# Kernel optimization log

Hardware: AMD Instinct MI355X
Metric: run time of the kernel (lower is better)

## Reference

```python
import jax, jax.numpy as jnp
import numpy as np
from jax import lax

TABLE_SIZE = 1024   # LSH table buckets
R = 2.5             # hash bucket width r
U = 0.83            # ALSH norm rescale bound
M = 9               # appended ALSH dims; M // (K*K) = 1 extra channel
K = 3               # kernel spatial size
PAD = 1


def _P(kflat, m):
    # L2-ALSH preprocessing: rescale so max row norm == U, append ||x||^{2^i}, i=1..m
    norms = jnp.linalg.norm(kflat, axis=1)
    x = kflat * (U / jnp.max(norms))
    p = jnp.sum(x * x, axis=1)  # ||x||^2
    powers = [p]
    for _ in range(m - 1):
        powers.append(powers[-1] ** 2)
    return jnp.concatenate([x, jnp.stack(powers, axis=1)], axis=1)  # [O, D+m]


def _conv(x, w):
    return lax.conv_general_dilated(
        x, w, window_strides=(1, 1), padding=[(PAD, PAD), (PAD, PAD)],
        dimension_numbers=("NCHW", "OIHW", "NCHW"))


def setup_inputs() -> dict:
    key = jax.random.key(0)
    k1, k2, k3, k4 = jax.random.split(key, 4)
    inp = jax.random.normal(k1, (16, 128, 64, 64), jnp.float32)
    kernels = jax.random.normal(k2, (256, 128, 3, 3), jnp.float32) * 0.05
    d = 128 + M // (K * K)  # 129
    a = jax.random.normal(k3, (d * K * K,), jnp.float32)  # 1161
    b = jax.random.uniform(k4, (1,), jnp.float32) * R
    return {"input": inp, "kernels": kernels, "a": a, "b": b}


def reference(input, kernels, a, b):
    O, C, kh, kw = kernels.shape
    B, _, H, W = input.shape
    extra_ch = M // (kh * kw)
    d = C + extra_ch

    # ---- init_table: hash every kernel row into a bucket ----
    kflat = kernels.reshape(O, -1)                       # [O, C*kh*kw]
    h = jnp.floor((_P(kflat, M) @ a + b[0]) / R)         # [O]
    bucket = jnp.abs(jnp.fmod(h.astype(jnp.int32), TABLE_SIZE))  # torch fmod+abs semantics

    # ---- vote: Q appends 0.5-filled channels, conv with hash vector as kernel ----
    input_Q = jnp.concatenate(
        [input, jnp.full((B, extra_ch, H, W), 0.5, input.dtype)], axis=1)
    dotted = _conv(input_Q, a.reshape(1, d, kh, kw))     # [B,1,H,W]
    votes = jnp.floor((dotted.reshape(-1) + b[0]) / R).astype(jnp.int32)
    vbucket = jnp.abs(jnp.fmod(votes, TABLE_SIZE))

    # ---- count_votes + argmax bucket ----
    count = jax.ops.segment_sum(jnp.ones(vbucket.shape, jnp.float32),
                                vbucket, num_segments=TABLE_SIZE)
    index = jnp.argmax(count)

    # ---- active set: kernels whose table bucket == winning bucket (mask form, jit-safe) ----
    mask = (bucket == index)                             # [O] bool
    active_kernels = kernels * mask[:, None, None, None].astype(kernels.dtype)

    # apply the active set (the conv this module feeds downstream)
    out = _conv(input, active_kernels)                   # [B,O,H,W]
    return out, index, mask
```

## Files before the change

### kernel.cpp

```cpp
#include <hip/hip_runtime.h>
#include <cmath>
#include <cstdint>

#define TSZ 1024
#define RDIV 2.5f
#define UCONST 0.83f

typedef __bf16 bf16x8 __attribute__((ext_vector_type(8)));
typedef float f32x4 __attribute__((ext_vector_type(4)));
typedef unsigned short ushortT;

__device__ __forceinline__ ushortT bf16r(float f) {
  union { float f; unsigned u; } x; x.f = f;
  unsigned r = (x.u + 0x7FFFu + ((x.u >> 16) & 1u)) >> 16;
  return (ushortT)r;
}

__device__ __forceinline__ void glds16(const void* g, void* l) {
  __builtin_amdgcn_global_load_lds(
      (const __attribute__((address_space(1))) unsigned int*)(g),
      (__attribute__((address_space(3))) unsigned int*)(l), 16, 0, 0);
}

__global__ __launch_bounds__(256) void k_cvtg(const float* __restrict__ in,
                                              const float* __restrict__ a,
                                              ushortT* __restrict__ nb,
                                              float* __restrict__ g) {
  __shared__ float tile2[64][129];
  __shared__ float gpart[4][9][64];
  const int bid = blockIdx.x;
  const int n = bid >> 6, y = bid & 63;
  const int t = threadIdx.x;
  {
    const int chs = t >> 4, l16 = t & 15;
    const float* basep = in + ((size_t)(n * 128) << 12) + (y << 6) + (l16 << 2);
#pragma unroll
    for (int i = 0; i < 8; ++i) {
      int ch = (i << 4) + chs;
      f32x4 v = *reinterpret_cast<const f32x4*>(basep + ((size_t)ch << 12));
#pragma unroll
      for (int u = 0; u < 4; ++u) tile2[(l16 << 2) + u][ch] = v[u];
    }
  }
  __syncthreads();
  {
    const int part = __builtin_amdgcn_readfirstlane(t >> 6);
    const int x = t & 63;
    float gacc[9];
#pragma unroll
    for (int tap = 0; tap < 9; ++tap) gacc[tap] = 0.f;
    const int c0 = part << 5;
#pragma unroll
    for (int i = 0; i < 32; ++i) {
      float v = tile2[x][c0 + i];
      const float* ap = a + (c0 + i) * 9;
#pragma unroll
      for (int tap = 0; tap < 9; ++tap) gacc[tap] += v * ap[tap];
    }
#pragma unroll
    for (int tap = 0; tap < 9; ++tap) gpart[part][tap][x] = gacc[tap];
  }
  __syncthreads();
  if (t < 64) {
    const int x = t;
#pragma unroll
    for (int tap = 0; tap < 9; ++tap) {
      float s = gpart[0][tap][x] + gpart[1][tap][x] + gpart[2][tap][x] + gpart[3][tap][x];
      g[tap * 65536 + (n << 12) + (y << 6) + x] = s;
    }
  }
  {
    const int x2 = t >> 2;
    ushortT* dst = nb + (((size_t)((n << 6) + y) << 6) + x2) * 128;
#pragma unroll
    for (int j = 0; j < 4; ++j) {
      int c0 = ((t & 3) << 3) + (j << 5);
      union { ushortT us[8]; uint4 v; } pk;
#pragma unroll
      for (int u = 0; u < 8; ++u) pk.us[u] = bf16r(tile2[x2][c0 + u]);
      *reinterpret_cast<uint4*>(dst + c0) = pk.v;
    }
  }
}

__global__ __launch_bounds__(256) void k_vote3(const float* __restrict__ g,
                                               const float* __restrict__ a,
                                               const float* __restrict__ bb,
                                               int* __restrict__ count) {
  __shared__ int hist[TSZ];
  const int t = threadIdx.x;
  for (int i = t; i < TSZ; i += 256) hist[i] = 0;
  __syncthreads();
  const int pix = blockIdx.x * 256 + t;
  const int n = pix >> 12, y = (pix >> 6) & 63, x = pix & 63;
  float acc = 0.f;
#pragma unroll
  for (int tap = 0; tap < 9; ++tap) {
    const int dy = tap / 3 - 1, dx = tap % 3 - 1;
    const int yy = y + dy, xx = x + dx;
    if ((unsigned)yy < 64u && (unsigned)xx < 64u)
      acc += g[tap * 65536 + (n << 12) + (yy << 6) + xx];
  }
  {
    const float* av = a + 1152;
#pragma unroll
    for (int ky = 0; ky < 3; ++ky) {
      int yy = y + ky - 1;
      if ((unsigned)yy >= 64u) continue;
#pragma unroll
      for (int kx = 0; kx < 3; ++kx) {
        int xx = x + kx - 1;
        if ((unsigned)xx >= 64u) continue;
        acc += 0.5f * av[ky * 3 + kx];
      }
    }
  }
  int v = (int)floorf((acc + bb[0]) / RDIV);
  int r = v % TSZ; if (r < 0) r = -r;
  atomicAdd(&hist[r], 1);
  __syncthreads();
  for (int i = t; i < TSZ; i += 256) {
    int h = hist[i];
    if (h) atomicAdd(&count[i], h);
  }
}

__global__ __launch_bounds__(256) void k_norm(const float* __restrict__ k,
                                              unsigned* __restrict__ scaleBits) {
  int o = blockIdx.x;
  const float* row = k + (size_t)o * 1152;
  float s = 0.f;
  for (int j = threadIdx.x; j < 1152; j += 256) { float v = row[j]; s += v * v; }
  __shared__ float red[256];
  red[threadIdx.x] = s; __syncthreads();
  for (int st = 128; st; st >>= 1) {
    if (threadIdx.x < st) red[threadIdx.x] += red[threadIdx.x + st];
    __syncthreads();
  }
  if (threadIdx.x == 0) atomicMax(scaleBits, __float_as_uint(red[0]));
}

__global__ __launch_bounds__(256) void k_hash(const float* __restrict__ k,
                                              const float* __restrict__ a,
                                              const float* __restrict__ b,
                                              const unsigned* __restrict__ scaleBits,
                                              int* __restrict__ bucket) {
  int o = blockIdx.x;
  float scale = UCONST / sqrtf(__uint_as_float(scaleBits[0]));
  const float* row = k + (size_t)o * 1152;
  float dot = 0.f, p = 0.f;
  for (int j = threadIdx.x; j < 1152; j += 256) {
    float x = row[j] * scale;
    dot += x * a[j];
    p += x * x;
  }
  __shared__ float rd[256], rp[256];
  rd[threadIdx.x] = dot; rp[threadIdx.x] = p; __syncthreads();
  for (int st = 128; st; st >>= 1) {
    if (threadIdx.x < st) { rd[threadIdx.x] += rd[threadIdx.x + st]; rp[threadIdx.x] += rp[threadIdx.x + st]; }
    __syncthreads();
  }
  if (threadIdx.x == 0) {
    float acc = rd[0];
    float pw = rp[0];
    for (int i = 0; i < 9; i++) { acc += pw * a[1152 + i]; pw = pw * pw; }
    acc += b[0];
    float h = floorf(acc / RDIV);
    int hi = (int)h;
    int r = hi % TSZ; if (r < 0) r = -r;
    bucket[o] = r;
  }
}

__global__ __launch_bounds__(256) void k_wprep2(const int* __restrict__ count,
                                                const int* __restrict__ bucket,
                                                const float* __restrict__ w,
                                                ushortT* __restrict__ wb,
                                                float* __restrict__ tail) {
  __shared__ int sc[256];
  __shared__ int si[256];
  const int t = threadIdx.x;
  int bc = count[t], bi = t;
#pragma unroll
  for (int j = 1; j < 4; ++j) {
    int i2 = t + j * 256;
    int c2 = count[i2];
    if (c2 > bc) { bc = c2; bi = i2; }
  }
  sc[t] = bc; si[t] = bi; __syncthreads();
  for (int st = 128; st; st >>= 1) {
    if (t < st) {
      int c2 = sc[t + st], i2 = si[t + st];
      if (c2 > sc[t] || (c2 == sc[t] && i2 < si[t])) { sc[t] = c2; si[t] = i2; }
    }
    __syncthreads();
  }
  const int idx = si[0];
  const int o = blockIdx.x;
  const int m = (bucket[o] == idx) ? 1 : 0;
  if (t == 0) {
    if (o == 0) tail[0] = (float)idx;
    tail[1 + o] = (float)m;
  }
  const float mf = m ? 1.f : 0.f;
  const float* wr = w + (size_t)o * 1152;
  ushortT* dst = wb + (size_t)o * 1152;
  for (int j = t; j < 1152; j += 256) {
    int r = j >> 7, c = j & 127;
    dst[j] = bf16r(wr[c * 9 + r] * mf);
  }
}

__global__ __launch_bounds__(512, 2) void k_gemm3r(const ushortT* __restrict__ nb,
                                                   const ushortT* __restrict__ wb,
                                                   const char* __restrict__ zp,
                                                   float* __restrict__ out) {
  __shared__ __align__(16) char smem[3 * 32768];
  const int t = threadIdx.x, l = t & 63, w = t >> 6;
  const int mb = blockIdx.x;
  const int n = mb >> 4;
  const int y0 = (mb & 15) << 2;
  const int wm = w & 1, wn = w >> 1;
  const int lr = l & 15, lq = l >> 4;
  const char* nbN = (const char*)nb + (size_t)n * 1048576;

  int cC[4], yA[4], xA[4];
  const char* bPj[4];
#pragma unroll
  for (int j = 0; j < 4; ++j) {
    int c = (w << 2) + j;
    cC[j] = c;
    int m = (c << 4) + lr;
    yA[j] = y0 + (m >> 6);
    xA[j] = m & 63;
    int orow = ((c - 16) << 4) + lr;
    bPj[j] = (const char*)wb + (size_t)orow * 2304 + (lq << 4);
  }

  auto stage = [&](int buf, int s) {
    const int tap = s >> 2;
    const int d3 = tap * 0x5556 >> 16;
    const int dy = d3 - 1, dx = tap - d3 * 3 - 1;
    const int cb = (s & 3) << 6;
    char* dstb = smem + buf * 32768;
#pragma unroll
    for (int j = 0; j < 4; ++j) {
      const char* src;
      if (cC[j] < 16) {
        int yy = yA[j] + dy, xx = xA[j] + dx;
        bool ok = ((unsigned)yy < 64u) && ((unsigned)xx < 64u);
        src = ok ? (nbN + (((yy << 6) + xx) << 8) + cb + (lq << 4))
                 : (zp + (lq << 4));
      } else {
        src = bPj[j] + (s << 6);
      }
      glds16(src, dstb + (cC[j] << 10));
    }
  };

  f32x4 acc[8][4] = {};

  stage(0, 0);
  stage(1, 1);
  asm volatile("s_waitcnt vmcnt(4)" ::: "memory");
  __builtin_amdgcn_s_barrier();

  for (int tt = 0; tt < 36; ++tt) {
    if (tt > 0) {
      if (tt < 35) { asm volatile("s_waitcnt vmcnt(4)" ::: "memory"); }
      else         { asm volatile("s_waitcnt vmcnt(0)" ::: "memory"); }
      __builtin_amdgcn_s_barrier();
    }
    if (tt + 2 < 36) stage((tt + 2) % 3, tt + 2);
    const char* bufb = smem + (tt % 3) * 32768;
    bf16x8 af[8], bv[4];
#pragma unroll
    for (int mi = 0; mi < 8; ++mi)
      af[mi] = *reinterpret_cast<const bf16x8*>(
          bufb + (((wm << 3) + mi) << 10) + (l << 4));
#pragma unroll
    for (int ni = 0; ni < 4; ++ni)
      bv[ni] = *reinterpret_cast<const bf16x8*>(
          bufb + 16384 + (((wn << 2) + ni) << 10) + (l << 4));
    __builtin_amdgcn_s_setprio(1);
#pragma unroll
    for (int mi = 0; mi < 8; ++mi)
#pragma unroll
      for (int ni = 0; ni < 4; ++ni)
        acc[mi][ni] = __builtin_amdgcn_mfma_f32_16x16x32_bf16(
            af[mi], bv[ni], acc[mi][ni], 0, 0, 0);
    __builtin_amdgcn_s_setprio(0);
  }

  const int pos0 = (mb & 15) << 8;
#pragma unroll
  for (int ni = 0; ni < 4; ++ni) {
    const int o = (wn << 6) + (ni << 4) + lr;
    float* op = out + ((size_t)((n << 8) + o) << 12) + pos0 + (wm << 7) + (lq << 2);
#pragma unroll
    for (int mi = 0; mi < 8; ++mi)
      *reinterpret_cast<f32x4*>(op + (mi << 4)) = acc[mi][ni];
  }
}

__global__ __launch_bounds__(256) void k_vote2(const float* __restrict__ in,
                                               const float* __restrict__ a,
                                               const float* __restrict__ bb,
                                               int* __restrict__ count) {
  __shared__ float sb[6][8][64];
  __shared__ int hist[TSZ];
  const int t = threadIdx.x;
  for (int i = t; i < TSZ; i += 256) hist[i] = 0;
  const int bid = blockIdx.x;
  const int n = bid >> 4, y0 = (bid & 15) << 2;
  const int x = t & 63, ry = t >> 6;
  const int yq = y0 + ry;
  float acc = 0.f;
  const float* base = in + (size_t)n * 524288;
  for (int cc = 0; cc < 16; ++cc) {
    __syncthreads();
#pragma unroll
    for (int k = 0; k < 12; ++k) {
      int i = k * 256 + t;
      int row = i >> 9;
      int c8 = (i >> 6) & 7;
      int xx = i & 63;
      int yy = y0 - 1 + row;
      float v = 0.f;
      if ((unsigned)yy < 64u) v = base[(size_t)(cc * 8 + c8) * 4096 + yy * 64 + xx];
      sb[row][c8][xx] = v;
    }
    __syncthreads();
#pragma unroll
    for (int c8 = 0; c8 < 8; ++c8) {
      const float* av = a + (cc * 8 + c8) * 9;
#pragma unroll
      for (int ky = 0; ky < 3; ++ky) {
        const float* rowp = sb[ry + ky][c8];
        float left  = (x >= 1)  ? rowp[x - 1] : 0.f;
        float mid   = rowp[x];
        float right = (x <= 62) ? rowp[x + 1] : 0.f;
        acc += left * av[ky * 3 + 0] + mid * av[ky * 3 + 1] + right * av[ky * 3 + 2];
      }
    }
  }
  {
    const float* av = a + 1152;
#pragma unroll
    for (int ky = 0; ky < 3; ++ky) {
      int yy = yq + ky - 1;
      if ((unsigned)yy >= 64u) continue;
#pragma unroll
      for (int kx = 0; kx < 3; ++kx) {
        int xx = x + kx - 1;
        if ((unsigned)xx >= 64u) continue;
        acc += 0.5f * av[ky * 3 + kx];
      }
    }
  }
  int v = (int)floorf((acc + bb[0]) / RDIV);
  int r = v % TSZ; if (r < 0) r = -r;
  atomicAdd(&hist[r], 1);
  __syncthreads();
  for (int i = t; i < TSZ; i += 256) {
    int h = hist[i];
    if (h) atomicAdd(&count[i], h);
  }
}

__global__ __launch_bounds__(1024) void k_argmax(const int* __restrict__ count,
                                                 const int* __restrict__ bucket,
                                                 int* __restrict__ maskI,
                                                 float* __restrict__ tail) {
  __shared__ int sc[1024];
  __shared__ int si[1024];
  int t = threadIdx.x;
  sc[t] = count[t]; si[t] = t; __syncthreads();
  for (int st = 512; st; st >>= 1) {
    if (t < st) {
      int c2 = sc[t + st], i2 = si[t + st];
      if (c2 > sc[t] || (c2 == sc[t] && i2 < si[t])) { sc[t] = c2; si[t] = i2; }
    }
    __syncthreads();
  }
  int idx = si[0];
  if (t == 0) tail[0] = (float)idx;
  if (t < 256) {
    int m = (bucket[t] == idx) ? 1 : 0;
    maskI[t] = m;
    tail[1 + t] = (float)m;
  }
}

__global__ __launch_bounds__(256) void k_conv(const float* __restrict__ in,
                                              const float* __restrict__ w,
                                              const int* __restrict__ maskI,
                                              float* __restrict__ out) {
  const int og = blockIdx.x, n = blockIdx.y, yt = blockIdx.z;
  const int tid = threadIdx.x;
  const int tx = tid & 63, trow = tid >> 6;
  const int y0 = yt * 4;
  const int oc0 = og * 4;
  const int m0 = maskI[oc0], m1 = maskI[oc0 + 1], m2 = maskI[oc0 + 2], m3 = maskI[oc0 + 3];
  float* op = out + ((size_t)(n * 256 + oc0)) * 4096 + (size_t)(y0 + trow) * 64 + tx;
  if (!(m0 | m1 | m2 | m3)) {
    op[0] = 0.f; op[4096] = 0.f; op[8192] = 0.f; op[12288] = 0.f;
    return;
  }
  __shared__ float tile[6 * 66];
  const float* base = in + (size_t)n * 128 * 4096;
  const float* wb = w + (size_t)oc0 * 1152;
  float a0 = 0.f, a1 = 0.f, a2 = 0.f, a3 = 0.f;
  for (int c = 0; c < 128; c++) {
    __syncthreads();
    for (int i = tid; i < 396; i += 256) {
      int r = i / 66, col = i - r * 66;
      int yy = y0 - 1 + r, xx = col - 1;
      float v = 0.f;
      if ((unsigned)yy < 64u && (unsigned)xx < 64u) v = base[(size_t)c * 4096 + yy * 64 + xx];
      tile[i] = v;
    }
    __syncthreads();
    const int ro = trow * 66 + tx;
    float t00 = tile[ro],        t01 = tile[ro + 1],   t02 = tile[ro + 2];
    float t10 = tile[ro + 66],   t11 = tile[ro + 67],  t12 = tile[ro + 68];
    float t20 = tile[ro + 132],  t21 = tile[ro + 133], t22 = tile[ro + 134];
    const float* wc = wb + c * 9;
    if (m0) { const float* q = wc;        a0 += t00*q[0]+t01*q[1]+t02*q[2]+t10*q[3]+t11*q[4]+t12*q[5]+t20*q[6]+t21*q[7]+t22*q[8]; }
    if (m1) { const float* q = wc + 1152; a1 += t00*q[0]+t01*q[1]+t02*q[2]+t10*q[3]+t11*q[4]+t12*q[5]+t20*q[6]+t21*q[7]+t22*q[8]; }
    if (m2) { const float* q = wc + 2304; a2 += t00*q[0]+t01*q[1]+t02*q[2]+t10*q[3]+t11*q[4]+t12*q[5]+t20*q[6]+t21*q[7]+t22*q[8]; }
    if (m3) { const float* q = wc + 3456; a3 += t00*q[0]+t01*q[1]+t02*q[2]+t10*q[3]+t11*q[4]+t12*q[5]+t20*q[6]+t21*q[7]+t22*q[8]; }
  }
  op[0]     = m0 ? a0 : 0.f;
  op[4096]  = m1 ? a1 : 0.f;
  op[8192]  = m2 ? a2 : 0.f;
  op[12288] = m3 ? a3 : 0.f;
}

extern "C" void kernel_launch(void* const* d_in, const int* in_sizes, int n_in,
                              void* d_out, int out_size, void* d_ws, size_t ws_size,
                              hipStream_t stream) {
  const float* in = (const float*)d_in[0];
  const float* kw = (const float*)d_in[1];
  const float* a  = (const float*)d_in[2];
  const float* b  = (const float*)d_in[3];
  float* out = (float*)d_out;

  char* ws = (char*)d_ws;
  const size_t NEED_BIG = 19731776ULL;

  if (ws_size >= NEED_BIG) {
    ushortT* nb   = (ushortT*)(ws);
    ushortT* wb   = (ushortT*)(ws + 16777216);
    float* g      = (float*)(ws + 17367040);
    int* count    = (int*)(ws + 19726336);
    unsigned* scB = (unsigned*)(ws + 19730432);
    char* zpage   = (ws + 19730496);
    int* bucket   = (int*)(ws + 19730752);

    hipMemsetAsync(ws + 19726336, 0, 4416, stream);

    k_norm<<<256, 256, 0, stream>>>(kw, scB);
    k_hash<<<256, 256, 0, stream>>>(kw, a, b, scB, bucket);
    k_cvtg<<<1024, 256, 0, stream>>>(in, a, nb, g);
    k_vote3<<<256, 256, 0, stream>>>(g, a, b, count);
    k_wprep2<<<256, 256, 0, stream>>>(count, bucket, kw, wb, out + 16777216);
    k_gemm3r<<<256, 512, 0, stream>>>(nb, wb, zpage, out);
  } else {
    int* count    = (int*)(ws);
    unsigned* scB = (unsigned*)(ws + 4096);
    int* bucket   = (int*)(ws + 4160);
    int* maskI    = (int*)(ws + 5184);

    hipMemsetAsync(ws, 0, 4160, stream);
    k_norm<<<256, 256, 0, stream>>>(kw, scB);
    k_hash<<<256, 256, 0, stream>>>(kw, a, b, scB, bucket);
    k_vote2<<<256, 256, 0, stream>>>(in, a, b, count);
    k_argmax<<<1, 1024, 0, stream>>>(count, bucket, maskI, out + 16777216);
    dim3 grid(64, 16, 16);
    k_conv<<<grid, 256, 0, stream>>>(in, kw, maskI, out);
  }
}
```

Measured before the change: 162.7 us.

## Split GEMM main loop into two half-phases interleaving staging with MFMA

The bf16 GEMM main loop now runs in two half-steps. Each half loads four A fragments, issues half of the next stage's global-to-LDS loads, waits at a barrier, then runs 16 MFMAs, so memory traffic interleaves with compute inside each iteration. Launch bounds drop to one block per SM. The conversion kernel's LDS tile is transposed to [128][65] and it now zeroes the vote count buffer, which shrinks the memset and moves k_cvtg ahead of the hash kernels. The extra barriers per iteration and the lower occupancy hint could offset the gain from overlap.

```diff
diff --git a/kernel.cpp b/kernel.cpp
--- a/kernel.cpp
+++ b/kernel.cpp
@@ -25,12 +25,14 @@
 __global__ __launch_bounds__(256) void k_cvtg(const float* __restrict__ in,
                                               const float* __restrict__ a,
                                               ushortT* __restrict__ nb,
-                                              float* __restrict__ g) {
-  __shared__ float tile2[64][129];
+                                              float* __restrict__ g,
+                                              int* __restrict__ count) {
+  __shared__ float tile2[128][65];
   __shared__ float gpart[4][9][64];
   const int bid = blockIdx.x;
   const int n = bid >> 6, y = bid & 63;
   const int t = threadIdx.x;
+  if (t == 0) count[bid] = 0;
   {
     const int chs = t >> 4, l16 = t & 15;
     const float* basep = in + ((size_t)(n * 128) << 12) + (y << 6) + (l16 << 2);
@@ -39,7 +41,7 @@
       int ch = (i << 4) + chs;
       f32x4 v = *reinterpret_cast<const f32x4*>(basep + ((size_t)ch << 12));
 #pragma unroll
-      for (int u = 0; u < 4; ++u) tile2[(l16 << 2) + u][ch] = v[u];
+      for (int u = 0; u < 4; ++u) tile2[ch][(l16 << 2) + u] = v[u];
     }
   }
   __syncthreads();
@@ -52,7 +54,7 @@
     const int c0 = part << 5;
 #pragma unroll
     for (int i = 0; i < 32; ++i) {
-      float v = tile2[x][c0 + i];
+      float v = tile2[c0 + i][x];
       const float* ap = a + (c0 + i) * 9;
 #pragma unroll
       for (int tap = 0; tap < 9; ++tap) gacc[tap] += v * ap[tap];
@@ -77,7 +79,7 @@
       int c0 = ((t & 3) << 3) + (j << 5);
       union { ushortT us[8]; uint4 v; } pk;
 #pragma unroll
-      for (int u = 0; u < 8; ++u) pk.us[u] = bf16r(tile2[x2][c0 + u]);
+      for (int u = 0; u < 8; ++u) pk.us[u] = bf16r(tile2[c0 + u][x2]);
       *reinterpret_cast<uint4*>(dst + c0) = pk.v;
     }
   }
@@ -211,10 +213,10 @@
   }
 }
 
-__global__ __launch_bounds__(512, 2) void k_gemm3r(const ushortT* __restrict__ nb,
-                                                   const ushortT* __restrict__ wb,
-                                                   const char* __restrict__ zp,
-                                                   float* __restrict__ out) {
+__global__ __launch_bounds__(512, 1) void k_gemm4(const ushortT* __restrict__ nb,
+                                                  const ushortT* __restrict__ wb,
+                                                  const char* __restrict__ zp,
+                                                  float* __restrict__ out) {
   __shared__ __align__(16) char smem[3 * 32768];
   const int t = threadIdx.x, l = t & 63, w = t >> 6;
   const int mb = blockIdx.x;
@@ -237,14 +239,14 @@
     bPj[j] = (const char*)wb + (size_t)orow * 2304 + (lq << 4);
   }
 
-  auto stage = [&](int buf, int s) {
+  auto stage2 = [&](int buf, int s, int jlo) {
     const int tap = s >> 2;
-    const int d3 = tap * 0x5556 >> 16;
+    const int d3 = (tap * 0x5556) >> 16;
     const int dy = d3 - 1, dx = tap - d3 * 3 - 1;
     const int cb = (s & 3) << 6;
     char* dstb = smem + buf * 32768;
 #pragma unroll
-    for (int j = 0; j < 4; ++j) {
+    for (int j = jlo; j < jlo + 2; ++j) {
       const char* src;
       if (cC[j] < 16) {
         int yy = yA[j] + dy, xx = xA[j] + dx;
@@ -260,36 +262,56 @@
 
   f32x4 acc[8][4] = {};
 
-  stage(0, 0);
-  stage(1, 1);
+  stage2(0, 0, 0); stage2(0, 0, 2);
+  stage2(1, 1, 0); stage2(1, 1, 2);
   asm volatile("s_waitcnt vmcnt(4)" ::: "memory");
   __builtin_amdgcn_s_barrier();
 
   for (int tt = 0; tt < 36; ++tt) {
-    if (tt > 0) {
-      if (tt < 35) { asm volatile("s_waitcnt vmcnt(4)" ::: "memory"); }
-      else         { asm volatile("s_waitcnt vmcnt(0)" ::: "memory"); }
-      __builtin_amdgcn_s_barrier();
-    }
-    if (tt + 2 < 36) stage((tt + 2) % 3, tt + 2);
     const char* bufb = smem + (tt % 3) * 32768;
-    bf16x8 af[8], bv[4];
-#pragma unroll
-    for (int mi = 0; mi < 8; ++mi)
-      af[mi] = *reinterpret_cast<const bf16x8*>(
-          bufb + (((wm << 3) + mi) << 10) + (l << 4));
+    const bool stg = (tt + 2) < 36;
+    const int sb = (tt + 2) % 3, ss = tt + 2;
+    bf16x8 bv[4], afA[4], afB[4];
 #pragma unroll
     for (int ni = 0; ni < 4; ++ni)
       bv[ni] = *reinterpret_cast<const bf16x8*>(
           bufb + 16384 + (((wn << 2) + ni) << 10) + (l << 4));
+#pragma unroll
+    for (int mi = 0; mi < 4; ++mi)
+      afA[mi] = *reinterpret_cast<const bf16x8*>(
+          bufb + (((wm << 3) + mi) << 10) + (l << 4));
+    if (stg) stage2(sb, ss, 0);
+    __builtin_amdgcn_s_barrier();
+    asm volatile("s_waitcnt lgkmcnt(0)" ::: "memory");
+    __builtin_amdgcn_sched_barrier(0);
     __builtin_amdgcn_s_setprio(1);
 #pragma unroll
-    for (int mi = 0; mi < 8; ++mi)
+    for (int mi = 0; mi < 4; ++mi)
 #pragma unroll
       for (int ni = 0; ni < 4; ++ni)
         acc[mi][ni] = __builtin_amdgcn_mfma_f32_16x16x32_bf16(
-            af[mi], bv[ni], acc[mi][ni], 0, 0, 0);
+            afA[mi], bv[ni], acc[mi][ni], 0, 0, 0);
     __builtin_amdgcn_s_setprio(0);
+    __builtin_amdgcn_s_barrier();
+#pragma unroll
+    for (int mi = 0; mi < 4; ++mi)
+      afB[mi] = *reinterpret_cast<const bf16x8*>(
+          bufb + (((wm << 3) + 4 + mi) << 10) + (l << 4));
+    if (stg) stage2(sb, ss, 2);
+    __builtin_amdgcn_s_barrier();
+    asm volatile("s_waitcnt lgkmcnt(0)" ::: "memory");
+    __builtin_amdgcn_sched_barrier(0);
+    __builtin_amdgcn_s_setprio(1);
+#pragma unroll
+    for (int mi = 0; mi < 4; ++mi)
+#pragma unroll
+      for (int ni = 0; ni < 4; ++ni)
+        acc[4 + mi][ni] = __builtin_amdgcn_mfma_f32_16x16x32_bf16(
+            afB[mi], bv[ni], acc[4 + mi][ni], 0, 0, 0);
+    __builtin_amdgcn_s_setprio(0);
+    if (tt < 35) asm volatile("s_waitcnt vmcnt(4)" ::: "memory");
+    else         asm volatile("s_waitcnt vmcnt(0)" ::: "memory");
+    __builtin_amdgcn_s_barrier();
   }
 
   const int pos0 = (mb & 15) << 8;
@@ -458,14 +480,14 @@
     char* zpage   = (ws + 19730496);
     int* bucket   = (int*)(ws + 19730752);
 
-    hipMemsetAsync(ws + 19726336, 0, 4416, stream);
-
+    hipMemsetAsync(ws + 19730432, 0, 320, stream);
+
+    k_cvtg<<<1024, 256, 0, stream>>>(in, a, nb, g, count);
     k_norm<<<256, 256, 0, stream>>>(kw, scB);
     k_hash<<<256, 256, 0, stream>>>(kw, a, b, scB, bucket);
-    k_cvtg<<<1024, 256, 0, stream>>>(in, a, nb, g);
     k_vote3<<<256, 256, 0, stream>>>(g, a, b, count);
     k_wprep2<<<256, 256, 0, stream>>>(count, bucket, kw, wb, out + 16777216);
-    k_gemm3r<<<256, 512, 0, stream>>>(nb, wb, zpage, out);
+    k_gemm4<<<256, 512, 0, stream>>>(nb, wb, zpage, out);
   } else {
     int* count    = (int*)(ws);
     unsigned* scB = (unsigned*)(ws + 4096);
```

Result: slower. 167.1 us (+2.7%).
